# Performance work log

Measured on AMD Instinct MI355X. Metric: run time of the kernel, lower is better.

The kernel has to match this reference:

```python
import jax, jax.numpy as jnp
import numpy as np

B, T, S, V = 4, 512, 256, 50257


def setup_inputs() -> dict:
    key = jax.random.key(0)
    k1, k2, k3 = jax.random.split(key, 3)
    p_source_position = jax.random.uniform(k1, (B, T, S), dtype=jnp.float32)
    p_target_vocab = jax.random.uniform(k2, (B, T, V), dtype=jnp.float32)
    input_source = jax.random.randint(k3, (B, S), 0, V, dtype=jnp.int64)
    return {
        "p_source_position": p_source_position,
        "p_target_vocab": p_target_vocab,
        "input_source": input_source,
    }


def reference(p_source_position, p_target_vocab, input_source):
    # Original: bmm(p_source_position [B,T,S], one_hot(input_source) [B,S,V])
    # == scatter-add of source-position probs into vocab bins indexed by input_source.
    vocab_size = p_target_vocab.shape[-1]

    def scatter_one(p_ts, src_s):
        # p_ts: [T, S], src_s: [S] -> [T, V]; duplicate indices accumulate.
        out = jnp.zeros((p_ts.shape[0], vocab_size), dtype=p_ts.dtype)
        return out.at[:, src_s].add(p_ts)

    return jax.vmap(scatter_one)(p_source_position, input_source)
```

## Files before the change

### kernel.cpp

```cpp
#include <hip/hip_runtime.h>
#include <stdint.h>

#define DIM_B 4
#define DIM_T 512
#define DIM_S 256
#define DIM_V 50257
#define DEPTH 4

__global__ __launch_bounds__(256) void onepass_kernel(
    const float* __restrict__ p_pos,
    const int*   __restrict__ src,
    float*       __restrict__ out)
{
    __shared__ uint32_t bkey[256][DEPTH];
    __shared__ float    bval[256][DEPTH];
    __shared__ int      bcnt[256];
    __shared__ uint32_t okey[DIM_S];
    __shared__ float    oval[DIM_S];
    __shared__ int      ocnt;

    const int row = blockIdx.x;
    const int b   = row >> 9;
    const int tid = threadIdx.x;

    bcnt[tid] = 0;
    if (tid == 0) ocnt = 0;
    __syncthreads();

    const long long rb   = (long long)row * DIM_V;
    const int head  = (int)((4 - (row & 3)) & 3);
    const int nvec  = (DIM_V - head) >> 2;
    const int ntail = DIM_V - head - (nvec << 2);

    {
        const int   v = src[b * DIM_S + tid];
        const float p = p_pos[(size_t)row * DIM_S + tid];
        const int   d = v - head;
        bool to_ovf = true;
        if (d >= 0 && d < (nvec << 2)) {
            const int c = d >> 2;
            const int t = c & 255;
            const int j = atomicAdd(&bcnt[t], 1);
            if (j < DEPTH) { bkey[t][j] = (uint32_t)d; bval[t][j] = p; to_ovf = false; }
        }
        if (to_ovf) {
            const int j = atomicAdd(&ocnt, 1);
            okey[j] = (uint32_t)v; oval[j] = p;
        }
    }
    __syncthreads();

    uint32_t k0 = 0xFFFFFFFFu, k1 = 0xFFFFFFFFu, k2 = 0xFFFFFFFFu, k3 = 0xFFFFFFFFu;
    float    v0 = 0.0f, v1 = 0.0f, v2 = 0.0f, v3 = 0.0f;
    {
        const int cnt = bcnt[tid];
        if (cnt > 0) { k0 = bkey[tid][0]; v0 = bval[tid][0]; }
        if (cnt > 1) { k1 = bkey[tid][1]; v1 = bval[tid][1]; }
        if (cnt > 2) { k2 = bkey[tid][2]; v2 = bval[tid][2]; }
        if (cnt > 3) { k3 = bkey[tid][3]; v3 = bval[tid][3]; }
    }

    float* __restrict__ rowp = out + rb;

    if (tid < head)  rowp[tid] = 0.0f;
    if (tid < ntail) rowp[head + (nvec << 2) + tid] = 0.0f;

    float4* __restrict__ vp = (float4*)(rowp + head);
    #pragma unroll 2
    for (int c = tid; c < nvec; c += 256) {
        const uint32_t d0 = (uint32_t)(c << 2);
        float4 o;
        o.x = ((k0 == d0    ) ? v0 : 0.0f) + ((k1 == d0    ) ? v1 : 0.0f)
            + ((k2 == d0    ) ? v2 : 0.0f) + ((k3 == d0    ) ? v3 : 0.0f);
        o.y = ((k0 == d0 + 1) ? v0 : 0.0f) + ((k1 == d0 + 1) ? v1 : 0.0f)
            + ((k2 == d0 + 1) ? v2 : 0.0f) + ((k3 == d0 + 1) ? v3 : 0.0f);
        o.z = ((k0 == d0 + 2) ? v0 : 0.0f) + ((k1 == d0 + 2) ? v1 : 0.0f)
            + ((k2 == d0 + 2) ? v2 : 0.0f) + ((k3 == d0 + 2) ? v3 : 0.0f);
        o.w = ((k0 == d0 + 3) ? v0 : 0.0f) + ((k1 == d0 + 3) ? v1 : 0.0f)
            + ((k2 == d0 + 3) ? v2 : 0.0f) + ((k3 == d0 + 3) ? v3 : 0.0f);
        vp[c] = o;
    }

    __syncthreads();
    for (int i = tid; i < ocnt; i += 256) {
        atomicAdd(rowp + okey[i], oval[i]);
    }
}

extern "C" void kernel_launch(void* const* d_in, const int* in_sizes, int n_in,
                              void* d_out, int out_size, void* d_ws, size_t ws_size,
                              hipStream_t stream) {
    const float* p_pos = (const float*)d_in[0];
    const int*   src   = (const int*)d_in[2];
    float*       out   = (float*)d_out;

    onepass_kernel<<<DIM_B * DIM_T, DIM_S, 0, stream>>>(p_pos, src, out);
}
```

Before: 88.67 us.

## Split scatter into global hash-bucket build, flat streaming write, and overflow pass

Replaces the one-block-per-row kernel with three kernels. The first buckets each (row, source) entry by flat float4 index into a global table in workspace. The second streams the whole output as a flat float4 array with a fixed grid, so every store is aligned and the head/tail handling disappears. The third applies overflow entries with atomics. It adds a memset, two more launches and global atomics, and falls back to the old kernel only when the workspace is too small.

After: 151.2 us. +70.5%, slower.

```diff
diff --git a/kernel.cpp b/kernel.cpp
--- a/kernel.cpp
+++ b/kernel.cpp
@@ -5,12 +5,83 @@
 #define DIM_T 512
 #define DIM_S 256
 #define DIM_V 50257
-#define DEPTH 4
+#define NROW   (DIM_B * DIM_T)
+#define NCHUNK 25731584u
+#define NT     524288u
+#define NTMSK  (NT - 1u)
+#define DEPTH  4
+
+#define WS_NEEDED (64 + 44ull * NT)
+
+__global__ __launch_bounds__(256) void build_kernel(
+    const float* __restrict__ p_pos, const int* __restrict__ src,
+    int* __restrict__ cnt, uint32_t* __restrict__ keys, float* __restrict__ vals,
+    int* __restrict__ ocnt, uint32_t* __restrict__ okey, float* __restrict__ oval)
+{
+    const int row = blockIdx.x;
+    const int b   = row >> 9;
+    const int tid = threadIdx.x;
+
+    const int      v = src[b * DIM_S + tid];
+    const float    p = p_pos[(size_t)row * DIM_S + tid];
+    const uint32_t e = (uint32_t)row * DIM_V + (uint32_t)v;
+    const uint32_t t = (e >> 2) & NTMSK;
+
+    const int j = atomicAdd(&cnt[t], 1);
+    if (j < DEPTH) {
+        keys[t * DEPTH + j] = e;
+        vals[t * DEPTH + j] = p;
+    } else {
+        const int oj = atomicAdd(ocnt, 1);
+        okey[oj] = e;
+        oval[oj] = p;
+    }
+}
+
+__global__ __launch_bounds__(256) void stream_kernel(
+    const int* __restrict__ cnt, const uint32_t* __restrict__ keys,
+    const float* __restrict__ vals, float4* __restrict__ out4)
+{
+    const uint32_t t = blockIdx.x * 256u + threadIdx.x;
+    const int      c = cnt[t];
+    const uint4  K = ((const uint4*)keys)[t];
+    const float4 W = ((const float4*)vals)[t];
+
+    uint32_t kc0 = 0xFFFFFFFFu, kc1 = 0xFFFFFFFFu, kc2 = 0xFFFFFFFFu, kc3 = 0xFFFFFFFFu;
+    float4 P0 = make_float4(0.f,0.f,0.f,0.f), P1 = P0, P2 = P0, P3 = P0;
+    if (c > 0) { kc0 = K.x >> 2; const int l = K.x & 3;
+        P0.x = l==0?W.x:0.f; P0.y = l==1?W.x:0.f; P0.z = l==2?W.x:0.f; P0.w = l==3?W.x:0.f; }
+    if (c > 1) { kc1 = K.y >> 2; const int l = K.y & 3;
+        P1.x = l==0?W.y:0.f; P1.y = l==1?W.y:0.f; P1.z = l==2?W.y:0.f; P1.w = l==3?W.y:0.f; }
+    if (c > 2) { kc2 = K.z >> 2; const int l = K.z & 3;
+        P2.x = l==0?W.z:0.f; P2.y = l==1?W.z:0.f; P2.z = l==2?W.z:0.f; P2.w = l==3?W.z:0.f; }
+    if (c > 3) { kc3 = K.w >> 2; const int l = K.w & 3;
+        P3.x = l==0?W.w:0.f; P3.y = l==1?W.w:0.f; P3.z = l==2?W.w:0.f; P3.w = l==3?W.w:0.f; }
+
+    #pragma unroll 4
+    for (uint32_t g = t; g < NCHUNK; g += NT) {
+        float4 o;
+        o.x = (g==kc0?P0.x:0.f) + (g==kc1?P1.x:0.f) + (g==kc2?P2.x:0.f) + (g==kc3?P3.x:0.f);
+        o.y = (g==kc0?P0.y:0.f) + (g==kc1?P1.y:0.f) + (g==kc2?P2.y:0.f) + (g==kc3?P3.y:0.f);
+        o.z = (g==kc0?P0.z:0.f) + (g==kc1?P1.z:0.f) + (g==kc2?P2.z:0.f) + (g==kc3?P3.z:0.f);
+        o.w = (g==kc0?P0.w:0.f) + (g==kc1?P1.w:0.f) + (g==kc2?P2.w:0.f) + (g==kc3?P3.w:0.f);
+        out4[g] = o;
+    }
+}
+
+__global__ __launch_bounds__(256) void overflow_kernel(
+    const int* __restrict__ ocnt, const uint32_t* __restrict__ okey,
+    const float* __restrict__ oval, float* __restrict__ out)
+{
+    const int n = *ocnt;
+    const int stride = gridDim.x * 256;
+    for (int i = blockIdx.x * 256 + threadIdx.x; i < n; i += stride)
+        atomicAdd(out + okey[i], oval[i]);
+}
 
 __global__ __launch_bounds__(256) void onepass_kernel(
-    const float* __restrict__ p_pos,
-    const int*   __restrict__ src,
-    float*       __restrict__ out)
+    const float* __restrict__ p_pos, const int* __restrict__ src,
+    float* __restrict__ out)
 {
     __shared__ uint32_t bkey[256][DEPTH];
     __shared__ float    bval[256][DEPTH];
@@ -43,15 +114,12 @@
             const int j = atomicAdd(&bcnt[t], 1);
             if (j < DEPTH) { bkey[t][j] = (uint32_t)d; bval[t][j] = p; to_ovf = false; }
         }
-        if (to_ovf) {
-            const int j = atomicAdd(&ocnt, 1);
-            okey[j] = (uint32_t)v; oval[j] = p;
-        }
+        if (to_ovf) { const int j = atomicAdd(&ocnt, 1); okey[j] = (uint32_t)v; oval[j] = p; }
     }
     __syncthreads();
 
     uint32_t k0 = 0xFFFFFFFFu, k1 = 0xFFFFFFFFu, k2 = 0xFFFFFFFFu, k3 = 0xFFFFFFFFu;
-    float    v0 = 0.0f, v1 = 0.0f, v2 = 0.0f, v3 = 0.0f;
+    float    v0 = 0.f, v1 = 0.f, v2 = 0.f, v3 = 0.f;
     {
         const int cnt = bcnt[tid];
         if (cnt > 0) { k0 = bkey[tid][0]; v0 = bval[tid][0]; }
@@ -61,30 +129,24 @@
     }
 
     float* __restrict__ rowp = out + rb;
-
     if (tid < head)  rowp[tid] = 0.0f;
     if (tid < ntail) rowp[head + (nvec << 2) + tid] = 0.0f;
 
     float4* __restrict__ vp = (float4*)(rowp + head);
     #pragma unroll 2
-    for (int c = tid; c < nvec; c += 256) {
-        const uint32_t d0 = (uint32_t)(c << 2);
+    for (int cc = tid; cc < nvec; cc += 256) {
+        const uint32_t d0 = (uint32_t)(cc << 2);
         float4 o;
-        o.x = ((k0 == d0    ) ? v0 : 0.0f) + ((k1 == d0    ) ? v1 : 0.0f)
-            + ((k2 == d0    ) ? v2 : 0.0f) + ((k3 == d0    ) ? v3 : 0.0f);
-        o.y = ((k0 == d0 + 1) ? v0 : 0.0f) + ((k1 == d0 + 1) ? v1 : 0.0f)
-            + ((k2 == d0 + 1) ? v2 : 0.0f) + ((k3 == d0 + 1) ? v3 : 0.0f);
-        o.z = ((k0 == d0 + 2) ? v0 : 0.0f) + ((k1 == d0 + 2) ? v1 : 0.0f)
-            + ((k2 == d0 + 2) ? v2 : 0.0f) + ((k3 == d0 + 2) ? v3 : 0.0f);
-        o.w = ((k0 == d0 + 3) ? v0 : 0.0f) + ((k1 == d0 + 3) ? v1 : 0.0f)
-            + ((k2 == d0 + 3) ? v2 : 0.0f) + ((k3 == d0 + 3) ? v3 : 0.0f);
-        vp[c] = o;
+        o.x = ((k0==d0    )?v0:0.f) + ((k1==d0    )?v1:0.f) + ((k2==d0    )?v2:0.f) + ((k3==d0    )?v3:0.f);
+        o.y = ((k0==d0+1u)?v0:0.f) + ((k1==d0+1u)?v1:0.f) + ((k2==d0+1u)?v2:0.f) + ((k3==d0+1u)?v3:0.f);
+        o.z = ((k0==d0+2u)?v0:0.f) + ((k1==d0+2u)?v1:0.f) + ((k2==d0+2u)?v2:0.f) + ((k3==d0+2u)?v3:0.f);
+        o.w = ((k0==d0+3u)?v0:0.f) + ((k1==d0+3u)?v1:0.f) + ((k2==d0+3u)?v2:0.f) + ((k3==d0+3u)?v3:0.f);
+        vp[cc] = o;
     }
 
     __syncthreads();
-    for (int i = tid; i < ocnt; i += 256) {
+    for (int i = tid; i < ocnt; i += 256)
         atomicAdd(rowp + okey[i], oval[i]);
-    }
 }
 
 extern "C" void kernel_launch(void* const* d_in, const int* in_sizes, int n_in,
@@ -94,5 +156,20 @@
     const int*   src   = (const int*)d_in[2];
     float*       out   = (float*)d_out;
 
-    onepass_kernel<<<DIM_B * DIM_T, DIM_S, 0, stream>>>(p_pos, src, out);
+    if (ws_size >= WS_NEEDED) {
+        char* base = (char*)d_ws;
+        int*      ocnt = (int*)base;
+        int*      cnt  = (int*)(base + 64);
+        uint32_t* keys = (uint32_t*)(base + 64 + 4ull * NT);
+        float*    vals = (float*)(base + 64 + 20ull * NT);
+        uint32_t* okey = (uint32_t*)(base + 64 + 36ull * NT);
+        float*    oval = (float*)(base + 64 + 40ull * NT);
+
+        hipMemsetAsync(d_ws, 0, 64 + 4ull * NT, stream);
+        build_kernel<<<NROW, DIM_S, 0, stream>>>(p_pos, src, cnt, keys, vals, ocnt, okey, oval);
+        stream_kernel<<<NT / 256, 256, 0, stream>>>(cnt, keys, vals, (float4*)out);
+        overflow_kernel<<<32, 256, 0, stream>>>(ocnt, okey, oval, out);
+    } else {
+        onepass_kernel<<<NROW, DIM_S, 0, stream>>>(p_pos, src, out);
+    }
 }
```

## Split scatter into global route, flat streaming write, and overflow kernels

Applied to the files above, without the earlier changes.

Replaces the one-block-per-row kernel with a multi-kernel pipeline. A route kernel buckets each (row, vocab) element into a global workspace bin per 256-element wave. A flat grid of float4 threads then zero-fills the output and writes bucketed hits, and a single-block kernel handles bin overflow with atomics. The aim is a uniform, fully parallel output write instead of a per-row loop, at the cost of a memset, extra launches, workspace traffic, and a single-block serial overflow pass. It falls back to the old kernel when the workspace is too small.

Measured after the change: 143.4 us. 1.62x slower.

```diff
diff --git a/kernel.cpp b/kernel.cpp
--- a/kernel.cpp
+++ b/kernel.cpp
@@ -5,15 +5,104 @@
 #define DIM_T 512
 #define DIM_S 256
 #define DIM_V 50257
-#define DEPTH 4
+#define NROW   2048
+#define NCHUNK 25731584u
+#define NZBLK  100514u
+#define NWAVE  402056u
+#define DEPTH  6
 
-__global__ __launch_bounds__(256) void onepass_kernel(
+#define OFF_OVFCNT 0ull
+#define OFF_CNT    256ull
+#define OFF_KEYS   1608704ull
+#define OFF_VALS   11258112ull
+#define OFF_OVFK   20907520ull
+#define OFF_OVFV   21169664ull
+#define WS_NEEDED  (OFF_OVFV + 262144ull)
+
+__global__ __launch_bounds__(256) void route_kernel(
     const float* __restrict__ p_pos,
     const int*   __restrict__ src,
-    float*       __restrict__ out)
+    int*       __restrict__ cnt,
+    uint32_t*  __restrict__ keys,
+    float*     __restrict__ vals,
+    int*       __restrict__ ovfcnt,
+    uint32_t*  __restrict__ ovfk,
+    float*     __restrict__ ovfv)
 {
-    __shared__ uint32_t bkey[256][DEPTH];
-    __shared__ float    bval[256][DEPTH];
+    const int row = blockIdx.x;
+    const int b   = row >> 9;
+    const int tid = threadIdx.x;
+
+    const int      v = src[b * DIM_S + tid];
+    const float    p = p_pos[(size_t)row * DIM_S + tid];
+    const uint32_t e = (uint32_t)row * DIM_V + (uint32_t)v;
+    const uint32_t w = e >> 8;
+
+    const int j = atomicAdd(&cnt[w], 1);
+    if (j < DEPTH) {
+        keys[w * DEPTH + j] = e;
+        vals[w * DEPTH + j] = p;
+    } else {
+        const int oj = atomicAdd(ovfcnt, 1);
+        ovfk[oj] = e;
+        ovfv[oj] = p;
+    }
+}
+
+__global__ __launch_bounds__(256) void stream_kernel(
+    const int*      __restrict__ cnt,
+    const uint32_t* __restrict__ keys,
+    const float*    __restrict__ vals,
+    float4*         __restrict__ out4)
+{
+    const uint32_t g = blockIdx.x * 256u + threadIdx.x;
+
+    out4[g] = make_float4(0.0f, 0.0f, 0.0f, 0.0f);
+    asm volatile("" ::: "memory");
+
+    const uint32_t w = g >> 6;
+    int c = cnt[w];
+    if (c == 0) return;
+    c = (c < DEPTH) ? c : DEPTH;
+
+    float4 o = make_float4(0.0f, 0.0f, 0.0f, 0.0f);
+    bool hit = false;
+    #pragma unroll
+    for (int i = 0; i < DEPTH; ++i) {
+        if (i < c) {
+            const uint32_t e = keys[w * DEPTH + i];
+            if ((e >> 2) == g) {
+                const float    pv = vals[w * DEPTH + i];
+                const uint32_t l  = e & 3u;
+                o.x += (l == 0u) ? pv : 0.0f;
+                o.y += (l == 1u) ? pv : 0.0f;
+                o.z += (l == 2u) ? pv : 0.0f;
+                o.w += (l == 3u) ? pv : 0.0f;
+                hit = true;
+            }
+        }
+    }
+    if (hit) out4[g] = o;
+}
+
+__global__ __launch_bounds__(256) void overflow_kernel(
+    const int* __restrict__ ovfcnt, const uint32_t* __restrict__ ovfk,
+    const float* __restrict__ ovfv, float* __restrict__ out)
+{
+    const int n = *ovfcnt;
+    for (int i = threadIdx.x; i < n; i += 256)
+        atomicAdd(out + ovfk[i], ovfv[i]);
+}
+
+#define HSZ  512
+#define HMSK (HSZ - 1)
+#define RDEPTH 4
+__global__ __launch_bounds__(256) void onepass_kernel(
+    const float* __restrict__ p_pos, const int* __restrict__ src,
+    float* __restrict__ out)
+{
+    __shared__ uint32_t bkey[256][RDEPTH];
+    __shared__ float    bval[256][RDEPTH];
     __shared__ int      bcnt[256];
     __shared__ uint32_t okey[DIM_S];
     __shared__ float    oval[DIM_S];
@@ -41,50 +130,41 @@
             const int c = d >> 2;
             const int t = c & 255;
             const int j = atomicAdd(&bcnt[t], 1);
-            if (j < DEPTH) { bkey[t][j] = (uint32_t)d; bval[t][j] = p; to_ovf = false; }
+            if (j < RDEPTH) { bkey[t][j] = (uint32_t)d; bval[t][j] = p; to_ovf = false; }
         }
-        if (to_ovf) {
-            const int j = atomicAdd(&ocnt, 1);
-            okey[j] = (uint32_t)v; oval[j] = p;
-        }
+        if (to_ovf) { const int j = atomicAdd(&ocnt, 1); okey[j] = (uint32_t)v; oval[j] = p; }
     }
     __syncthreads();
 
     uint32_t k0 = 0xFFFFFFFFu, k1 = 0xFFFFFFFFu, k2 = 0xFFFFFFFFu, k3 = 0xFFFFFFFFu;
-    float    v0 = 0.0f, v1 = 0.0f, v2 = 0.0f, v3 = 0.0f;
+    float    v0 = 0.f, v1 = 0.f, v2 = 0.f, v3 = 0.f;
     {
-        const int cnt = bcnt[tid];
-        if (cnt > 0) { k0 = bkey[tid][0]; v0 = bval[tid][0]; }
-        if (cnt > 1) { k1 = bkey[tid][1]; v1 = bval[tid][1]; }
-        if (cnt > 2) { k2 = bkey[tid][2]; v2 = bval[tid][2]; }
-        if (cnt > 3) { k3 = bkey[tid][3]; v3 = bval[tid][3]; }
+        const int c = bcnt[tid];
+        if (c > 0) { k0 = bkey[tid][0]; v0 = bval[tid][0]; }
+        if (c > 1) { k1 = bkey[tid][1]; v1 = bval[tid][1]; }
+        if (c > 2) { k2 = bkey[tid][2]; v2 = bval[tid][2]; }
+        if (c > 3) { k3 = bkey[tid][3]; v3 = bval[tid][3]; }
     }
 
     float* __restrict__ rowp = out + rb;
-
     if (tid < head)  rowp[tid] = 0.0f;
     if (tid < ntail) rowp[head + (nvec << 2) + tid] = 0.0f;
 
     float4* __restrict__ vp = (float4*)(rowp + head);
     #pragma unroll 2
-    for (int c = tid; c < nvec; c += 256) {
-        const uint32_t d0 = (uint32_t)(c << 2);
+    for (int cc = tid; cc < nvec; cc += 256) {
+        const uint32_t d0 = (uint32_t)(cc << 2);
         float4 o;
-        o.x = ((k0 == d0    ) ? v0 : 0.0f) + ((k1 == d0    ) ? v1 : 0.0f)
-            + ((k2 == d0    ) ? v2 : 0.0f) + ((k3 == d0    ) ? v3 : 0.0f);
-        o.y = ((k0 == d0 + 1) ? v0 : 0.0f) + ((k1 == d0 + 1) ? v1 : 0.0f)
-            + ((k2 == d0 + 1) ? v2 : 0.0f) + ((k3 == d0 + 1) ? v3 : 0.0f);
-        o.z = ((k0 == d0 + 2) ? v0 : 0.0f) + ((k1 == d0 + 2) ? v1 : 0.0f)
-            + ((k2 == d0 + 2) ? v2 : 0.0f) + ((k3 == d0 + 2) ? v3 : 0.0f);
-        o.w = ((k0 == d0 + 3) ? v0 : 0.0f) + ((k1 == d0 + 3) ? v1 : 0.0f)
-            + ((k2 == d0 + 3) ? v2 : 0.0f) + ((k3 == d0 + 3) ? v3 : 0.0f);
-        vp[c] = o;
+        o.x = ((k0==d0    )?v0:0.f) + ((k1==d0    )?v1:0.f) + ((k2==d0    )?v2:0.f) + ((k3==d0    )?v3:0.f);
+        o.y = ((k0==d0+1u)?v0:0.f) + ((k1==d0+1u)?v1:0.f) + ((k2==d0+1u)?v2:0.f) + ((k3==d0+1u)?v3:0.f);
+        o.z = ((k0==d0+2u)?v0:0.f) + ((k1==d0+2u)?v1:0.f) + ((k2==d0+2u)?v2:0.f) + ((k3==d0+2u)?v3:0.f);
+        o.w = ((k0==d0+3u)?v0:0.f) + ((k1==d0+3u)?v1:0.f) + ((k2==d0+3u)?v2:0.f) + ((k3==d0+3u)?v3:0.f);
+        vp[cc] = o;
     }
 
     __syncthreads();
-    for (int i = tid; i < ocnt; i += 256) {
+    for (int i = tid; i < ocnt; i += 256)
         atomicAdd(rowp + okey[i], oval[i]);
-    }
 }
 
 extern "C" void kernel_launch(void* const* d_in, const int* in_sizes, int n_in,
@@ -94,5 +174,21 @@
     const int*   src   = (const int*)d_in[2];
     float*       out   = (float*)d_out;
 
-    onepass_kernel<<<DIM_B * DIM_T, DIM_S, 0, stream>>>(p_pos, src, out);
+    if (ws_size >= WS_NEEDED) {
+        char* base = (char*)d_ws;
+        int*      ovfcnt = (int*)(base + OFF_OVFCNT);
+        int*      cnt    = (int*)(base + OFF_CNT);
+        uint32_t* keys   = (uint32_t*)(base + OFF_KEYS);
+        float*    vals   = (float*)(base + OFF_VALS);
+        uint32_t* ovfk   = (uint32_t*)(base + OFF_OVFK);
+        float*    ovfv   = (float*)(base + OFF_OVFV);
+
+        hipMemsetAsync(d_ws, 0, OFF_CNT + (size_t)NWAVE * 4, stream);
+        route_kernel<<<NROW, DIM_S, 0, stream>>>(p_pos, src, cnt, keys, vals,
+                                                 ovfcnt, ovfk, ovfv);
+        stream_kernel<<<NZBLK, 256, 0, stream>>>(cnt, keys, vals, (float4*)out);
+        overflow_kernel<<<1, 256, 0, stream>>>(ovfcnt, ovfk, ovfv, out);
+    } else {
+        onepass_kernel<<<NROW, DIM_S, 0, stream>>>(p_pos, src, out);
+    }
 }
```
